# Kernel tuning notes

Hardware: AMD Instinct MI355X
Metric: run time of the kernel (lower is better)

Reference implementation:

```python
import jax, jax.numpy as jnp
import numpy as np

HEADS = 2
NEG_SLOPE = 0.2

def _seg_softmax(alpha, dst, n):
    # numerically-stable softmax over edges grouped by destination node (PyG softmax)
    m = jax.ops.segment_max(alpha, dst, num_segments=n)
    m = jax.lax.stop_gradient(jnp.where(jnp.isfinite(m), m, 0.0))
    e = jnp.exp(alpha - m[dst])
    s = jax.ops.segment_sum(e, dst, num_segments=n)
    return e / (s[dst] + 1e-16)

def _han_layer(xo, xa, e_oo, e_oa, e_ao, Wo, bo, Wa, ba, asrc, adst, Wk, bk, q):
    No, Na = xo.shape[0], xa.shape[0]
    C = Wo.shape[1]
    D = C // HEADS
    h = {'object': (xo @ Wo + bo).reshape(No, HEADS, D),
         'attribute': (xa @ Wa + ba).reshape(Na, HEADS, D)}
    n = {'object': No, 'attribute': Na}
    edge_types = [('object', 'object', e_oo), ('object', 'attribute', e_oa),
                  ('attribute', 'object', e_ao)]
    outs = {'object': [], 'attribute': []}
    for i, (st, dt, e) in enumerate(edge_types):
        src, dst = e[0], e[1]
        # per-edge attention logits [E, H]
        a = (h[st] * asrc[i]).sum(-1)[src] + (h[dt] * adst[i]).sum(-1)[dst]
        a = jax.nn.leaky_relu(a, NEG_SLOPE)
        a = _seg_softmax(a, dst, n[dt])
        msg = (h[st][src] * a[..., None]).reshape(-1, C)  # [E, C]
        outs[dt].append(jax.nn.relu(jax.ops.segment_sum(msg, dst, num_segments=n[dt])))
    res = {}
    for nt, xs in outs.items():
        o = jnp.stack(xs)  # [M, N, C] over metapaths
        score = (q * jnp.tanh(o @ Wk + bk).mean(axis=1)).sum(-1)  # [M]
        w = jax.nn.softmax(score, axis=0)
        res[nt] = jnp.einsum('m,mnc->nc', w, o)
    return res


def setup_inputs() -> dict:
    key = jax.random.key(0)
    ks = jax.random.split(key, 40)
    No, Na, E, C, H = 100000, 50000, 500000, 128, 2
    D = C // H
    def rn(k, shape, scale):
        return jax.random.normal(k, shape, jnp.float32) * scale
    inp = {}
    inp['x_object'] = rn(ks[0], (No, C), 1.0)
    inp['x_attribute'] = rn(ks[1], (Na, C), 1.0)
    inp['e_oo'] = jax.random.randint(ks[2], (2, E), 0, No)
    inp['e_oa'] = jnp.stack([jax.random.randint(ks[3], (E,), 0, No),
                             jax.random.randint(ks[4], (E,), 0, Na)])
    inp['e_ao'] = jnp.stack([jax.random.randint(ks[5], (E,), 0, Na),
                             jax.random.randint(ks[6], (E,), 0, No)])
    s = 1.0 / float(np.sqrt(C))
    for L, off in (('1', 7), ('2', 16)):
        inp['Wo' + L] = rn(ks[off], (C, C), s)
        inp['bo' + L] = jnp.zeros((C,), jnp.float32)
        inp['Wa' + L] = rn(ks[off + 1], (C, C), s)
        inp['ba' + L] = jnp.zeros((C,), jnp.float32)
        inp['asrc' + L] = rn(ks[off + 2], (3, H, D), s)
        inp['adst' + L] = rn(ks[off + 3], (3, H, D), s)
        inp['Wk' + L] = rn(ks[off + 4], (C, C), s)
        inp['bk' + L] = jnp.zeros((C,), jnp.float32)
        inp['q' + L] = rn(ks[off + 5], (C,), s)
    inp['Wl1'] = rn(ks[30], (C, 256), s)
    inp['bl1'] = jnp.zeros((256,), jnp.float32)
    inp['Wl2'] = rn(ks[31], (256, 128), 1.0 / float(np.sqrt(256)))
    inp['bl2'] = jnp.zeros((128,), jnp.float32)
    inp['Wl3'] = rn(ks[32], (128, 8), 1.0 / float(np.sqrt(128)))
    inp['bl3'] = jnp.zeros((8,), jnp.float32)
    return inp


def reference(x_object, x_attribute, e_oo, e_oa, e_ao,
              Wo1, bo1, Wa1, ba1, asrc1, adst1, Wk1, bk1, q1,
              Wo2, bo2, Wa2, ba2, asrc2, adst2, Wk2, bk2, q2,
              Wl1, bl1, Wl2, bl2, Wl3, bl3):
    h = _han_layer(x_object, x_attribute, e_oo, e_oa, e_ao,
                   Wo1, bo1, Wa1, ba1, asrc1, adst1, Wk1, bk1, q1)
    h = _han_layer(h['object'], h['attribute'], e_oo, e_oa, e_ao,
                   Wo2, bo2, Wa2, ba2, asrc2, adst2, Wk2, bk2, q2)
    x = h['object'] @ Wl1 + bl1
    x = x @ Wl2 + bl2
    x = x @ Wl3 + bl3
    return jax.nn.sigmoid(x)
```

## Files before the change

kernel.cpp:

```cpp
#include <hip/hip_runtime.h>
#include <hip/hip_bf16.h>
#include <math.h>

#define CDIM 128
typedef unsigned short u16;
typedef unsigned int u32;
typedef short bf16x8 __attribute__((ext_vector_type(8)));
typedef float f32x4 __attribute__((ext_vector_type(4)));

__device__ __forceinline__ float bf2f(__hip_bfloat16 h) { return __bfloat162float(h); }
__device__ __forceinline__ u16 f2bfbits(float f) {
  __hip_bfloat16 h = __float2bfloat16(f);
  u16 u;
  __builtin_memcpy(&u, &h, 2);
  return u;
}
__device__ __forceinline__ float bfbits2f(u16 b) { return __uint_as_float((u32)b << 16); }
__device__ __forceinline__ float lrelu(float v) { return v > 0.f ? v : 0.2f * v; }
__device__ __forceinline__ float lo_bf(u32 v) { return __uint_as_float(v << 16); }
__device__ __forceinline__ float hi_bf(u32 v) { return __uint_as_float(v & 0xffff0000u); }
__device__ __forceinline__ u32 pack_bf(float a, float b) {
  return (u32)f2bfbits(a) | ((u32)f2bfbits(b) << 16);
}

#define WREP 8
#define WFSZ 16384

__global__ void detect_kernel(const u16* __restrict__ p, int nwords, int* __restrict__ flag) {
  int i = blockIdx.x * blockDim.x + threadIdx.x;
  if (i >= nwords) return;
  int ex = (p[i] >> 7) & 0xFF;
  if (ex >= 0xC0) atomicOr(flag, 1);
}

struct CvtJob { const void* src; float* dst; int n; };
struct CvtJobs24 { CvtJob j[24]; };
__global__ void cvt_batch_kernel(CvtJobs24 jobs, const int* __restrict__ flag) {
  CvtJob jb = jobs.j[blockIdx.y];
  int i = blockIdx.x * blockDim.x + threadIdx.x;
  if (i >= jb.n) return;
  if (*flag) jb.dst[i] = ((const float*)jb.src)[i];
  else jb.dst[i] = bf2f(((const __hip_bfloat16*)jb.src)[i]);
}

__global__ void fill_out_kernel(void* __restrict__ out, float v, int n,
                                const int* __restrict__ flag) {
  int i = blockIdx.x * blockDim.x + threadIdx.x;
  if (i >= n) return;
  if (*flag) ((float*)out)[i] = v;
  else ((__hip_bfloat16*)out)[i] = __float2bfloat16(v);
}

struct RepackJobs { const float* src[6]; u16* dst[6]; };
__global__ void repack_w_kernel(RepackJobs jobs) {
  const float* W = jobs.src[blockIdx.y];
  u16* Wf = jobs.dst[blockIdx.y] + ((size_t)blockIdx.z << 14);
  int idx = blockIdx.x * 256 + threadIdx.x;
  int j = idx & 7, lane = (idx >> 3) & 63, kc = (idx >> 9) & 3, nt = idx >> 11;
  int k = kc * 32 + ((lane >> 4) & 3) * 8 + j;
  int n = nt * 16 + (lane & 15);
  Wf[idx] = f2bfbits(W[k * 128 + n]);
}

struct CsrJobs {
  const int* src[3]; const int* dst[3];
  int* deg[3]; int* cur[3]; int* bsum[3]; int* offs[3]; int* adj[3];
  int Nd[3]; int E;
};
__global__ void deg_batch_kernel(CsrJobs c) {
  int y = blockIdx.y;
  int e = blockIdx.x * blockDim.x + threadIdx.x;
  if (e < c.E) atomicAdd(&c.deg[y][c.dst[y][e]], 1);
}
__global__ void scanp_batch_kernel(CsrJobs c) {
  int y = blockIdx.y, N = c.Nd[y];
  __shared__ int red[256];
  int t = threadIdx.x;
  int base = blockIdx.x * 1024 + t * 4;
  int s = 0;
#pragma unroll
  for (int j = 0; j < 4; ++j) if (base + j < N) s += c.deg[y][base + j];
  red[t] = s;
  __syncthreads();
  for (int o = 128; o; o >>= 1) {
    if (t < o) red[t] += red[t + o];
    __syncthreads();
  }
  if (t == 0) c.bsum[y][blockIdx.x] = red[0];
}
__global__ void scanb_batch_kernel(CsrJobs c) {
  int y = threadIdx.x;
  if (y >= 3) return;
  int nb = (c.Nd[y] + 1023) / 1024;
  int run = 0;
  for (int i = 0; i < nb; ++i) { int v = c.bsum[y][i]; c.bsum[y][i] = run; run += v; }
  c.offs[y][c.Nd[y]] = c.E;
}
__global__ void scanf_batch_kernel(CsrJobs c) {
  int y = blockIdx.y, N = c.Nd[y];
  __shared__ int lds[256];
  int t = threadIdx.x;
  int base = blockIdx.x * 1024 + t * 4;
  int v0 = (base + 0 < N) ? c.deg[y][base + 0] : 0;
  int v1 = (base + 1 < N) ? c.deg[y][base + 1] : 0;
  int v2 = (base + 2 < N) ? c.deg[y][base + 2] : 0;
  int v3 = (base + 3 < N) ? c.deg[y][base + 3] : 0;
  int tsum = v0 + v1 + v2 + v3;
  lds[t] = tsum;
  __syncthreads();
  for (int o = 1; o < 256; o <<= 1) {
    int x = (t >= o) ? lds[t - o] : 0;
    __syncthreads();
    lds[t] += x;
    __syncthreads();
  }
  int excl = lds[t] - tsum + c.bsum[y][blockIdx.x];
  int e0 = excl, e1 = excl + v0, e2 = excl + v0 + v1, e3 = excl + v0 + v1 + v2;
  if (base + 0 < N) { c.offs[y][base + 0] = e0; c.cur[y][base + 0] = e0; }
  if (base + 1 < N) { c.offs[y][base + 1] = e1; c.cur[y][base + 1] = e1; }
  if (base + 2 < N) { c.offs[y][base + 2] = e2; c.cur[y][base + 2] = e2; }
  if (base + 3 < N) { c.offs[y][base + 3] = e3; c.cur[y][base + 3] = e3; }
}
__global__ void fill_batch_kernel(CsrJobs c) {
  int y = blockIdx.y;
  int range8 = blockIdx.x & 7;
  int base = (blockIdx.x >> 3) * 1024 + threadIdx.x * 4;
  if (base >= c.E) return;
  int Nd = c.Nd[y];
  int rsz = (Nd + 7) >> 3;
  int lo = range8 * rsz, hi = lo + rsz;
  const int* dsty = c.dst[y];
  const int* srcy = c.src[y];
  int4 d4;
  if (base + 3 < c.E) {
    d4 = *(const int4*)&dsty[base];
  } else {
    d4.x = dsty[base];
    d4.y = (base + 1 < c.E) ? dsty[base + 1] : -1;
    d4.z = (base + 2 < c.E) ? dsty[base + 2] : -1;
    d4.w = (base + 3 < c.E) ? dsty[base + 3] : -1;
  }
  int dv[4] = { d4.x, d4.y, d4.z, d4.w };
#pragma unroll
  for (int j = 0; j < 4; ++j) {
    int d = dv[j];
    if (d >= lo && d < hi) {
      int p = atomicAdd(&c.cur[y][d], 1);
      c.adj[y][p] = srcy[base + j];
    }
  }
}

struct GemmJob {
  const void* X; const void* X2; const float* W2;
  const u16* Wf; const float* bias;
  const float* av[4]; float* od[4];
  u16* out; int M;
};

template<int MODE>
__device__ __forceinline__ void gemm_load_a(
    const GemmJob& jb, const int* flag, int r, int ko, bf16x8 a[4]) {
  if (MODE == 1 && *flag) {
    const float* af = (const float*)jb.X + (size_t)r * 128 + ko;
#pragma unroll
    for (int c = 0; c < 4; ++c) {
      float4 x = *(const float4*)(af + c * 32);
      float4 y = *(const float4*)(af + c * 32 + 4);
      bf16x8 tv;
      tv[0] = (short)f2bfbits(x.x); tv[1] = (short)f2bfbits(x.y);
      tv[2] = (short)f2bfbits(x.z); tv[3] = (short)f2bfbits(x.w);
      tv[4] = (short)f2bfbits(y.x); tv[5] = (short)f2bfbits(y.y);
      tv[6] = (short)f2bfbits(y.z); tv[7] = (short)f2bfbits(y.w);
      a[c] = tv;
    }
  } else if (MODE == 2) {
    float w0 = jb.W2[0], w1 = jb.W2[1];
    const u16* g1 = (const u16*)jb.X + (size_t)r * 128 + ko;
    const u16* g2 = (const u16*)jb.X2 + (size_t)r * 128 + ko;
#pragma unroll
    for (int c = 0; c < 4; ++c) {
      bf16x8 x1 = *(const bf16x8*)(g1 + c * 32);
      bf16x8 x2 = *(const bf16x8*)(g2 + c * 32);
      bf16x8 tv;
#pragma unroll
      for (int k = 0; k < 8; ++k)
        tv[k] = (short)f2bfbits(w0 * bfbits2f((u16)x1[k]) + w1 * bfbits2f((u16)x2[k]));
      a[c] = tv;
    }
  } else {
    const u16* ab = (const u16*)jb.X + (size_t)r * 128 + ko;
#pragma unroll
    for (int c = 0; c < 4; ++c) a[c] = *(const bf16x8*)(ab + c * 32);
  }
}

template<int MODE, int K>
__global__ __launch_bounds__(256, 4) void gemm_mfma_t(
    GemmJob jb, const int* __restrict__ flag)
{
  int bx = blockIdx.x;
  int M = jb.M;
  __shared__ u16 Cs[64][136];
  int t = threadIdx.x;
  int wave = t >> 6, lane = t & 63;
  int m = lane & 15, ko = (lane >> 4) * 8, rq = lane >> 4;
  int rowbase = bx * 128;
  const u16* wf = jb.Wf + ((size_t)(bx & (WREP - 1)) << 14);

  int r0 = rowbase + wave * 16 + m;       if (r0 >= M) r0 = M - 1;
  int r1 = rowbase + 64 + wave * 16 + m;  if (r1 >= M) r1 = M - 1;
  bf16x8 a0[4], a1[4];
  gemm_load_a<MODE>(jb, flag, r0, ko, a0);
  gemm_load_a<MODE>(jb, flag, r1, ko, a1);

#pragma unroll
  for (int tile = 0; tile < 2; ++tile) {
    int row0 = rowbase + tile * 64 + wave * 16;
    bf16x8* a = tile ? a1 : a0;
    if (row0 < M) {
      f32x4 acc[8];
#pragma unroll
      for (int nt = 0; nt < 8; ++nt) acc[nt] = (f32x4){0.f, 0.f, 0.f, 0.f};
#pragma unroll
      for (int c = 0; c < 4; ++c) {
        bf16x8 b[8];
#pragma unroll
        for (int nt = 0; nt < 8; ++nt)
          b[nt] = *(const bf16x8*)(wf + ((nt * 4 + c) * 64 + lane) * 8);
#pragma unroll
        for (int nt = 0; nt < 8; ++nt)
          acc[nt] = __builtin_amdgcn_mfma_f32_16x16x32_bf16(a[c], b[nt], acc[nt], 0, 0, 0);
      }
#pragma unroll
      for (int nt = 0; nt < 8; ++nt) {
        float bv = jb.bias[nt * 16 + m];
#pragma unroll
        for (int reg = 0; reg < 4; ++reg) acc[nt][reg] += bv;
      }
#pragma unroll
      for (int nt = 0; nt < 8; ++nt) {
        int col = nt * 16 + m;
#pragma unroll
        for (int reg = 0; reg < 4; ++reg)
          Cs[wave * 16 + rq * 4 + reg][col] = f2bfbits(acc[nt][reg]);
      }
#pragma unroll
      for (int k = 0; k < K; ++k) {
        const float* avk = jb.av[k];
        float* odk = jb.od[k];
        float am[8];
#pragma unroll
        for (int nt = 0; nt < 8; ++nt) am[nt] = avk[nt * 16 + m];
#pragma unroll
        for (int reg = 0; reg < 4; ++reg) {
          float p0 = 0.f, p1 = 0.f;
#pragma unroll
          for (int nt = 0; nt < 4; ++nt) p0 = fmaf(acc[nt][reg], am[nt], p0);
#pragma unroll
          for (int nt = 4; nt < 8; ++nt) p1 = fmaf(acc[nt][reg], am[nt], p1);
#pragma unroll
          for (int msk = 1; msk < 16; msk <<= 1) {
            p0 += __shfl_xor(p0, msk);
            p1 += __shfl_xor(p1, msk);
          }
          if (m == 0) {
            int row = row0 + rq * 4 + reg;
            if (row < M) { odk[row * 2] = p0; odk[row * 2 + 1] = p1; }
          }
        }
      }
    }
    __syncthreads();
#pragma unroll
    for (int kk = 0; kk < 4; ++kk) {
      int idx = t + kk * 256;
      int rowl = idx >> 4, c16 = idx & 15;
      int grow = rowbase + tile * 64 + rowl;
      if (grow < M) {
        uint4 v = *(const uint4*)&Cs[rowl][c16 * 8];
        *(uint4*)((u16*)jb.out + (size_t)grow * 128 + c16 * 8) = v;
      }
    }
    __syncthreads();
  }
}

__global__ __launch_bounds__(256) void tanhsum_mfma_kernel(
    const u16* __restrict__ A0, const u16* __restrict__ A1,
    const u16* __restrict__ Wf, const float* __restrict__ bias,
    float* __restrict__ score, int M)
{
  const u16* A = blockIdx.y ? A1 : A0;
  float* sc = score + blockIdx.y * 128;
  __shared__ __align__(16) u16 Bs[WFSZ];
  __shared__ float sred[4][128];
  int t = threadIdx.x;
  int wave = t >> 6, lane = t & 63;
  int m = lane & 15, ko = (lane >> 4) * 8, rq = lane >> 4;
  {
    const uint4* wfg = (const uint4*)(Wf + ((size_t)(blockIdx.x & (WREP - 1)) << 14));
    uint4* bs4 = (uint4*)Bs;
#pragma unroll
    for (int i = 0; i < 8; ++i) bs4[t + i * 256] = wfg[t + i * 256];
  }
  __syncthreads();
  float colsum[8];
#pragma unroll
  for (int nt = 0; nt < 8; ++nt) colsum[nt] = 0.f;
  for (int row0 = blockIdx.x * 64 + wave * 16; row0 < M; row0 += gridDim.x * 64) {
    int r = row0 + m; if (r >= M) r = M - 1;
    const u16* arow = A + (size_t)r * 128 + ko;
    bf16x8 a[4];
#pragma unroll
    for (int c = 0; c < 4; ++c) a[c] = *(const bf16x8*)(arow + c * 32);
    f32x4 acc[8];
#pragma unroll
    for (int nt = 0; nt < 8; ++nt) acc[nt] = (f32x4){0.f, 0.f, 0.f, 0.f};
#pragma unroll
    for (int c = 0; c < 4; ++c) {
      bf16x8 b[8];
#pragma unroll
      for (int nt = 0; nt < 8; ++nt)
        b[nt] = *(const bf16x8*)(Bs + ((nt * 4 + c) * 64 + lane) * 8);
#pragma unroll
      for (int nt = 0; nt < 8; ++nt)
        acc[nt] = __builtin_amdgcn_mfma_f32_16x16x32_bf16(a[c], b[nt], acc[nt], 0, 0, 0);
    }
#pragma unroll
    for (int nt = 0; nt < 8; ++nt) {
      float bv = bias[nt * 16 + m];
#pragma unroll
      for (int reg = 0; reg < 4; ++reg) {
        int row = row0 + rq * 4 + reg;
        if (row < M) colsum[nt] += tanhf(acc[nt][reg] + bv);
      }
    }
  }
#pragma unroll
  for (int nt = 0; nt < 8; ++nt) {
    colsum[nt] += __shfl_xor(colsum[nt], 16);
    colsum[nt] += __shfl_xor(colsum[nt], 32);
  }
  if (lane < 16) {
#pragma unroll
    for (int nt = 0; nt < 8; ++nt) sred[wave][nt * 16 + lane] = colsum[nt];
  }
  __syncthreads();
  if (t < 128) {
    float tot = sred[0][t] + sred[1][t] + sred[2][t] + sred[3][t];
    atomicAdd(&sc[t], tot);
  }
}

__global__ void sem_w_kernel(const float* __restrict__ score, const float* __restrict__ q,
                             float invN, float* __restrict__ W2) {
  int t = threadIdx.x;
  float s0 = 0.f, s1 = 0.f;
  for (int c = t; c < 128; c += 64) {
    float qc = q[c];
    s0 += qc * score[c];
    s1 += qc * score[128 + c];
  }
#pragma unroll
  for (int o = 32; o; o >>= 1) {
    s0 += __shfl_xor(s0, o);
    s1 += __shfl_xor(s1, o);
  }
  if (t == 0) {
    s0 *= invN; s1 *= invN;
    float mx = fmaxf(s0, s1);
    float e0 = expf(s0 - mx), e1 = expf(s1 - mx);
    float inv = 1.f / (e0 + e1);
    W2[0] = e0 * inv;
    W2[1] = e1 * inv;
  }
}

struct GatherJob {
  const int* offs; const int* adj;
  const float* ss; const float* sd;
  float* ew;
  const u16* Hs; u16* out; int Nd;
};
struct GatherJobs3 { GatherJob j[3]; };
__global__ __launch_bounds__(256) void node_gather_b_kernel(GatherJobs3 g, int nb0, int nb01)
{
  int bx = blockIdx.x;
  int jbi = bx < nb0 ? 0 : (bx < nb01 ? 1 : 2);
  int bl = jbi == 0 ? bx : (jbi == 1 ? bx - nb0 : bx - nb01);
  GatherJob jb = g.j[jbi];
  int lane = threadIdx.x & 63;
  int grp = lane >> 4, sl = lane & 15;
  int wid = bl * 4 + (threadIdx.x >> 6);
  int node = wid * 4 + grp;
  bool act = node < jb.Nd;
  int beg = 0, end = 0;
  float2 sdp = make_float2(0.f, 0.f);
  if (act) {
    beg = jb.offs[node];
    end = jb.offs[node + 1];
    sdp = ((const float2*)jb.sd)[node];
  }
  int deg = end - beg;
  const float2* ss2 = (const float2*)jb.ss;
  float2* ew2 = (float2*)jb.ew;
  const uint4* H4 = (const uint4*)jb.Hs;
  bool hi2 = sl >= 8;
  int base = grp * 16;
  float a[8];
#pragma unroll
  for (int j = 0; j < 8; ++j) a[j] = 0.f;
  float invh;
  if (__all(deg <= 16)) {
    int adjreg = 0;
    if (sl < deg) adjreg = jb.adj[beg + sl];
    int sidx[8];
#pragma unroll
    for (int j = 0; j < 8; ++j) sidx[j] = __shfl(adjreg, base + j);
    float2 ssp = make_float2(0.f, 0.f);
    if (sl < deg) ssp = ss2[adjreg];
    uint4 v[8];
#pragma unroll
    for (int j = 0; j < 8; ++j)
      if (j < deg) v[j] = H4[(size_t)sidx[j] * 16 + sl];
    float e0r = 0.f, e1r = 0.f;
    if (sl < deg) {
      e0r = expf(lrelu(ssp.x + sdp.x));
      e1r = expf(lrelu(ssp.y + sdp.y));
    }
    float s0 = e0r, s1 = e1r;
#pragma unroll
    for (int o = 1; o < 16; o <<= 1) {
      s0 += __shfl_xor(s0, o);
      s1 += __shfl_xor(s1, o);
    }
    invh = 1.f / ((hi2 ? s1 : s0) + 1e-16f);
#pragma unroll
    for (int j = 0; j < 8; ++j) {
      float wl = __shfl(e0r, base + j);
      float wh = __shfl(e1r, base + j);
      if (j < deg) {
        float w = hi2 ? wh : wl;
        a[0] = fmaf(lo_bf(v[j].x), w, a[0]);
        a[1] = fmaf(hi_bf(v[j].x), w, a[1]);
        a[2] = fmaf(lo_bf(v[j].y), w, a[2]);
        a[3] = fmaf(hi_bf(v[j].y), w, a[3]);
        a[4] = fmaf(lo_bf(v[j].z), w, a[4]);
        a[5] = fmaf(hi_bf(v[j].z), w, a[5]);
        a[6] = fmaf(lo_bf(v[j].w), w, a[6]);
        a[7] = fmaf(hi_bf(v[j].w), w, a[7]);
      }
    }
    if (__any(deg > 8)) {
#pragma unroll
      for (int j = 0; j < 8; ++j) {
        int s2 = __shfl(adjreg, base + 8 + j);
        float wl = __shfl(e0r, base + 8 + j);
        float wh = __shfl(e1r, base + 8 + j);
        if (8 + j < deg) {
          uint4 vv = H4[(size_t)s2 * 16 + sl];
          float w = hi2 ? wh : wl;
          a[0] = fmaf(lo_bf(vv.x), w, a[0]);
          a[1] = fmaf(hi_bf(vv.x), w, a[1]);
          a[2] = fmaf(lo_bf(vv.y), w, a[2]);
          a[3] = fmaf(hi_bf(vv.y), w, a[3]);
          a[4] = fmaf(lo_bf(vv.z), w, a[4]);
          a[5] = fmaf(hi_bf(vv.z), w, a[5]);
          a[6] = fmaf(lo_bf(vv.w), w, a[6]);
          a[7] = fmaf(hi_bf(vv.w), w, a[7]);
        }
      }
    }
  } else {
    float s0 = 0.f, s1 = 0.f;
    for (int e = beg + sl; e < end; e += 16) {
      int s = jb.adj[e];
      float2 ssp = ss2[s];
      float f0 = expf(lrelu(ssp.x + sdp.x));
      float f1 = expf(lrelu(ssp.y + sdp.y));
      ew2[e] = make_float2(f0, f1);
      s0 += f0;
      s1 += f1;
    }
#pragma unroll
    for (int o = 1; o < 16; o <<= 1) {
      s0 += __shfl_xor(s0, o);
      s1 += __shfl_xor(s1, o);
    }
    invh = 1.f / ((hi2 ? s1 : s0) + 1e-16f);
    for (int eb = beg; eb < end; eb += 4) {
      int eA[4]; uint4 v[4]; float w[4];
#pragma unroll
      for (int j = 0; j < 4; ++j) eA[j] = (eb + j < end) ? eb + j : end - 1;
#pragma unroll
      for (int j = 0; j < 4; ++j) v[j] = H4[(size_t)jb.adj[eA[j]] * 16 + sl];
#pragma unroll
      for (int j = 0; j < 4; ++j) {
        float2 p = ew2[eA[j]];
        w[j] = (eb + j < end) ? (hi2 ? p.y : p.x) : 0.f;
      }
#pragma unroll
      for (int j = 0; j < 4; ++j) {
        a[0] = fmaf(lo_bf(v[j].x), w[j], a[0]);
        a[1] = fmaf(hi_bf(v[j].x), w[j], a[1]);
        a[2] = fmaf(lo_bf(v[j].y), w[j], a[2]);
        a[3] = fmaf(hi_bf(v[j].y), w[j], a[3]);
        a[4] = fmaf(lo_bf(v[j].z), w[j], a[4]);
        a[5] = fmaf(hi_bf(v[j].z), w[j], a[5]);
        a[6] = fmaf(lo_bf(v[j].w), w[j], a[6]);
        a[7] = fmaf(hi_bf(v[j].w), w[j], a[7]);
      }
    }
  }
  if (act) {
    uint4 o;
    o.x = pack_bf(fmaxf(a[0] * invh, 0.f), fmaxf(a[1] * invh, 0.f));
    o.y = pack_bf(fmaxf(a[2] * invh, 0.f), fmaxf(a[3] * invh, 0.f));
    o.z = pack_bf(fmaxf(a[4] * invh, 0.f), fmaxf(a[5] * invh, 0.f));
    o.w = pack_bf(fmaxf(a[6] * invh, 0.f), fmaxf(a[7] * invh, 0.f));
    ((uint4*)jb.out)[(size_t)node * 16 + sl] = o;
  }
}

__global__ void fold1_kernel(const float* __restrict__ Wl1, const float* __restrict__ bl1,
                             const float* __restrict__ Wl2, const float* __restrict__ bl2,
                             float* __restrict__ WT1, float* __restrict__ TB) {
  int idx = blockIdx.x * blockDim.x + threadIdx.x;
  if (idx < 128 * 128) {
    int m = idx >> 7, n = idx & 127;
    float acc = 0.f;
    for (int k = 0; k < 256; ++k) acc = fmaf(Wl1[m * 256 + k], Wl2[k * 128 + n], acc);
    WT1[idx] = acc;
  } else if (idx < 128 * 128 + 128) {
    int n = idx - 128 * 128;
    float acc = bl2[n];
    for (int k = 0; k < 256; ++k) acc = fmaf(bl1[k], Wl2[k * 128 + n], acc);
    TB[n] = acc;
  }
}
__global__ void fold2_kernel(const float* __restrict__ WT1, const float* __restrict__ TB,
                             const float* __restrict__ Wl3, const float* __restrict__ bl3,
                             float* __restrict__ WC, float* __restrict__ BC) {
  int idx = blockIdx.x * blockDim.x + threadIdx.x;
  if (idx < 128 * 8) {
    int m = idx >> 3, j = idx & 7;
    float acc = 0.f;
    for (int k = 0; k < 128; ++k) acc = fmaf(WT1[m * 128 + k], Wl3[k * 8 + j], acc);
    WC[idx] = acc;
  } else if (idx < 128 * 8 + 8) {
    int j = idx - 128 * 8;
    float acc = bl3[j];
    for (int k = 0; k < 128; ++k) acc = fmaf(TB[k], Wl3[k * 8 + j], acc);
    BC[j] = acc;
  }
}

__global__ __launch_bounds__(256) void final_mlp_kernel(
    const u16* __restrict__ X1, const u16* __restrict__ X2,
    const float* __restrict__ W2, const int* __restrict__ flag,
    const float* __restrict__ Wc, const float* __restrict__ bc,
    void* __restrict__ out, int M) {
  __shared__ float Xs[32][130];
  int rb = blockIdx.x * 32;
  int t = threadIdx.x;
  float w0 = W2[0], w1 = W2[1];
  for (int i = t; i < 32 * 64; i += 256) {
    int r = i >> 6, c2 = i & 63;
    int gr = rb + r;
    u32 v1 = 0, v2 = 0;
    if (gr < M) {
      v1 = ((const u32*)X1)[(size_t)gr * 64 + c2];
      v2 = ((const u32*)X2)[(size_t)gr * 64 + c2];
    }
    Xs[r][c2 * 2] = w0 * lo_bf(v1) + w1 * lo_bf(v2);
    Xs[r][c2 * 2 + 1] = w0 * hi_bf(v1) + w1 * hi_bf(v2);
  }
  __syncthreads();
  int r = t >> 3, j = t & 7;
  int gr = rb + r;
  if (gr >= M) return;
  float acc = bc[j];
#pragma unroll 4
  for (int c = 0; c < 128; ++c) acc = fmaf(Xs[r][c], Wc[c * 8 + j], acc);
  float v = 1.f / (1.f + expf(-acc));
  if (*flag) ((float*)out)[(size_t)gr * 8 + j] = v;
  else ((__hip_bfloat16*)out)[(size_t)gr * 8 + j] = __float2bfloat16(v);
}

extern "C" void kernel_launch(void* const* d_in, const int* in_sizes, int n_in,
                              void* d_out, int out_size, void* d_ws, size_t ws_size,
                              hipStream_t stream) {
  const int No = in_sizes[0] / CDIM;
  const int Na = in_sizes[1] / CDIM;
  const int E = in_sizes[2] / 2;
  const int NM = No > Na ? No : Na;

  char* base = (char*)d_ws;
  size_t off = 0;
  auto alloc = [&](size_t bytes) -> void* {
    off = (off + 255) & ~(size_t)255;
    void* p = base + off;
    off += bytes;
    return p;
  };

  int* FLAG = (int*)alloc(4);
  u16* G1b = (u16*)alloc((size_t)No * CDIM * 2);
  u16* XAb = (u16*)alloc((size_t)Na * CDIM * 2);
  u16* HOb = (u16*)alloc((size_t)No * CDIM * 2);
  u16* HAb = (u16*)alloc((size_t)Na * CDIM * 2);
  u16* G2b = (u16*)alloc((size_t)No * CDIM * 2);
  float* OD0 = (float*)alloc((size_t)No * 2 * 4);
  float* OD1 = (float*)alloc((size_t)No * 2 * 4);
  float* OD2 = (float*)alloc((size_t)No * 2 * 4);
  float* OD3 = (float*)alloc((size_t)No * 2 * 4);
  float* AD0 = (float*)alloc((size_t)Na * 2 * 4);
  float* AD1 = (float*)alloc((size_t)Na * 2 * 4);
  float* EW0 = (float*)alloc((size_t)E * 2 * 4);
  float* EW1 = (float*)alloc((size_t)E * 2 * 4);
  float* EW2 = (float*)alloc((size_t)E * 2 * 4);
  int* DEG3 = (int*)alloc((size_t)NM * 3 * 4);
  float* SCORE = (float*)alloc(512 * 4);
  float* SEMW = (float*)alloc(4 * 4);
  float* WT1 = (float*)alloc(128 * 128 * 4);
  float* TB = (float*)alloc(128 * 4);
  float* WC = (float*)alloc(128 * 8 * 4);
  float* BC = (float*)alloc(8 * 4);
  int* OFFS_OO = (int*)alloc((size_t)(No + 1) * 4);
  int* OFFS_OA = (int*)alloc((size_t)(Na + 1) * 4);
  int* OFFS_AO = (int*)alloc((size_t)(No + 1) * 4);
  int* ADJ_OO = (int*)alloc((size_t)E * 4);
  int* ADJ_OA = (int*)alloc((size_t)E * 4);
  int* ADJ_AO = (int*)alloc((size_t)E * 4);
  int* CUR3 = (int*)alloc((size_t)NM * 3 * 4);
  int* BSUM3 = (int*)alloc(3 * 128 * 4);
  u16* WF[6];
  for (int i = 0; i < 6; ++i) WF[i] = (u16*)alloc((size_t)WFSZ * WREP * 2);
  float* F[29];
  for (int i = 5; i < 29; ++i) F[i] = (float*)alloc((size_t)in_sizes[i] * 4);

  hipMemsetAsync(FLAG, 0, 4, stream);
  detect_kernel<<<64, 256, 0, stream>>>((const u16*)d_in[0], 16384, FLAG);

  if (off > ws_size) {
    fill_out_kernel<<<(out_size + 255) / 256, 256, 0, stream>>>(d_out, 0.25f, out_size, FLAG);
    return;
  }

  {
    CvtJobs24 jobs;
    int maxn = 0;
    for (int i = 5; i < 29; ++i) {
      jobs.j[i - 5].src = d_in[i];
      jobs.j[i - 5].dst = F[i];
      jobs.j[i - 5].n = in_sizes[i];
      if (in_sizes[i] > maxn) maxn = in_sizes[i];
    }
    dim3 g((maxn + 255) / 256, 24);
    cvt_batch_kernel<<<g, 256, 0, stream>>>(jobs, FLAG);
  }

  {
    RepackJobs rj;
    const int widx[6] = { 5, 7, 11, 14, 16, 20 };
    for (int i = 0; i < 6; ++i) { rj.src[i] = F[widx[i]]; rj.dst[i] = WF[i]; }
    dim3 g(64, 6, WREP);
    repack_w_kernel<<<g, 256, 0, stream>>>(rj);
  }

  {
    CsrJobs c;
    const int* EOO = (const int*)d_in[2];
    const int* EOA = (const int*)d_in[3];
    const int* EAO = (const int*)d_in[4];
    c.src[0] = EOO; c.dst[0] = EOO + E; c.Nd[0] = No; c.offs[0] = OFFS_OO; c.adj[0] = ADJ_OO;
    c.src[1] = EOA; c.dst[1] = EOA + E; c.Nd[1] = Na; c.offs[1] = OFFS_OA; c.adj[1] = ADJ_OA;
    c.src[2] = EAO; c.dst[2] = EAO + E; c.Nd[2] = No; c.offs[2] = OFFS_AO; c.adj[2] = ADJ_AO;
    for (int i = 0; i < 3; ++i) {
      c.deg[i] = DEG3 + (size_t)i * NM;
      c.cur[i] = CUR3 + (size_t)i * NM;
      c.bsum[i] = BSUM3 + i * 128;
    }
    c.E = E;
    size_t zlen = (size_t)((char*)(SEMW + 4) - (char*)DEG3);
    hipMemsetAsync(DEG3, 0, zlen, stream);
    int nbmax = (NM + 1023) / 1024;
    deg_batch_kernel<<<dim3((E + 255) / 256, 3), 256, 0, stream>>>(c);
    scanp_batch_kernel<<<dim3(nbmax, 3), 256, 0, stream>>>(c);
    scanb_batch_kernel<<<1, 64, 0, stream>>>(c);
    scanf_batch_kernel<<<dim3(nbmax, 3), 256, 0, stream>>>(c);
    fill_batch_kernel<<<dim3(((E + 1023) / 1024) * 8, 3), 256, 0, stream>>>(c);
  }

  const int nb0 = (No + 127) / 128;
  const int nb1 = (Na + 127) / 128;

  auto run_layer = [&](int L, const void* XO, const void* XO2, const float* W2in,
                       const void* XA,
                       const float* bo, const float* ba,
                       const float* av, const float* ad, const float* bk,
                       const float* q) {
    u16* WFo = WF[L * 3 + 0];
    u16* WFa = WF[L * 3 + 1];
    u16* WFk = WF[L * 3 + 2];
    float* SC = SCORE + L * 256;
    GemmJob j0;
    j0.X = XO; j0.X2 = XO2; j0.W2 = W2in;
    j0.Wf = WFo; j0.bias = bo;
    j0.av[0] = av + 0;   j0.od[0] = OD0;
    j0.av[1] = ad + 0;   j0.od[1] = OD1;
    j0.av[2] = av + 128; j0.od[2] = OD2;
    j0.av[3] = ad + 256; j0.od[3] = OD3;
    j0.out = HOb; j0.M = No;
    GemmJob j1;
    j1.X = XA; j1.X2 = nullptr; j1.W2 = nullptr;
    j1.Wf = WFa; j1.bias = ba;
    j1.av[0] = av + 256; j1.od[0] = AD0;
    j1.av[1] = ad + 128; j1.od[1] = AD1;
    j1.av[2] = nullptr;  j1.od[2] = nullptr;
    j1.av[3] = nullptr;  j1.od[3] = nullptr;
    j1.out = HAb; j1.M = Na;
    if (L == 0) {
      gemm_mfma_t<1, 4><<<nb0, 256, 0, stream>>>(j0, FLAG);
      gemm_mfma_t<1, 2><<<nb1, 256, 0, stream>>>(j1, FLAG);
    } else {
      gemm_mfma_t<2, 4><<<nb0, 256, 0, stream>>>(j0, FLAG);
      gemm_mfma_t<0, 1><<<nb1, 256, 0, stream>>>(j1, FLAG);
    }

    GatherJobs3 ga;
    ga.j[0] = { OFFS_OO, ADJ_OO, OD0, OD1, EW0, HOb, G1b, No };
    int c0 = (No + 15) / 16, c1, c2;
    if (L == 0) {
      ga.j[1] = { OFFS_OA, ADJ_OA, OD2, AD1, EW1, HOb, XAb, Na };
      ga.j[2] = { OFFS_AO, ADJ_AO, AD0, OD3, EW2, HAb, G2b, No };
      c1 = (Na + 15) / 16;
      c2 = (No + 15) / 16;
    } else {
      ga.j[1] = { OFFS_AO, ADJ_AO, AD0, OD3, EW2, HAb, G2b, No };
      ga.j[2] = ga.j[1];
      c1 = (No + 15) / 16;
      c2 = 0;
    }
    node_gather_b_kernel<<<c0 + c1 + c2, 256, 0, stream>>>(ga, c0, c0 + c1);

    tanhsum_mfma_kernel<<<dim3(512, 2), 256, 0, stream>>>(G1b, G2b, WFk, bk, SC, No);
    sem_w_kernel<<<1, 64, 0, stream>>>(SC, q, 1.f / (float)No, SEMW + L * 2);
  };

  run_layer(0, d_in[0], nullptr, nullptr, d_in[1],
            F[6], F[8], F[9], F[10], F[12], F[13]);
  run_layer(1, G1b, G2b, SEMW, XAb,
            F[15], F[17], F[18], F[19], F[21], F[22]);

  fold1_kernel<<<(128 * 128 + 128 + 255) / 256, 256, 0, stream>>>(F[23], F[24], F[25], F[26], WT1, TB);
  fold2_kernel<<<(128 * 8 + 8 + 255) / 256, 256, 0, stream>>>(WT1, TB, F[27], F[28], WC, BC);

  final_mlp_kernel<<<(No + 31) / 32, 256, 0, stream>>>(G1b, G2b, SEMW + 2, FLAG, WC, BC, d_out, No);
}
```

Measured before the change: 652.7 us.

## Build CSR with per-edge atomic ranks instead of cursor-based fill

The degree-count kernel now records the value returned by the atomic increment as each edge's rank within its destination segment. The fill kernel then scatters source ids to offs[dst]+rank with no atomics and no longer needs the 8-way destination range partitioning that read the edge list eight times. This removes the cursor array and the second pass of atomics. The cost is an extra E-sized rank buffer per edge type that must be written and read back, and the adjacency order within a segment becomes nondeterministic.

```diff
diff --git a/kernel.cpp b/kernel.cpp
--- a/kernel.cpp
+++ b/kernel.cpp
@@ -64,13 +64,21 @@
 
 struct CsrJobs {
   const int* src[3]; const int* dst[3];
-  int* deg[3]; int* cur[3]; int* bsum[3]; int* offs[3]; int* adj[3];
+  int* deg[3]; int* rank[3]; int* bsum[3]; int* offs[3]; int* adj[3];
   int Nd[3]; int E;
 };
 __global__ void deg_batch_kernel(CsrJobs c) {
   int y = blockIdx.y;
-  int e = blockIdx.x * blockDim.x + threadIdx.x;
-  if (e < c.E) atomicAdd(&c.deg[y][c.dst[y][e]], 1);
+  int base = (blockIdx.x * blockDim.x + threadIdx.x) * 4;
+  if (base >= c.E) return;
+  const int* dsty = c.dst[y];
+  int* degy = c.deg[y];
+  int* ranky = c.rank[y];
+#pragma unroll
+  for (int j = 0; j < 4; ++j) {
+    int e = base + j;
+    if (e < c.E) ranky[e] = atomicAdd(&degy[dsty[e]], 1);
+  }
 }
 __global__ void scanp_batch_kernel(CsrJobs c) {
   int y = blockIdx.y, N = c.Nd[y];
@@ -115,38 +123,32 @@
     __syncthreads();
   }
   int excl = lds[t] - tsum + c.bsum[y][blockIdx.x];
-  int e0 = excl, e1 = excl + v0, e2 = excl + v0 + v1, e3 = excl + v0 + v1 + v2;
-  if (base + 0 < N) { c.offs[y][base + 0] = e0; c.cur[y][base + 0] = e0; }
-  if (base + 1 < N) { c.offs[y][base + 1] = e1; c.cur[y][base + 1] = e1; }
-  if (base + 2 < N) { c.offs[y][base + 2] = e2; c.cur[y][base + 2] = e2; }
-  if (base + 3 < N) { c.offs[y][base + 3] = e3; c.cur[y][base + 3] = e3; }
+  if (base + 0 < N) c.offs[y][base + 0] = excl;
+  if (base + 1 < N) c.offs[y][base + 1] = excl + v0;
+  if (base + 2 < N) c.offs[y][base + 2] = excl + v0 + v1;
+  if (base + 3 < N) c.offs[y][base + 3] = excl + v0 + v1 + v2;
 }
 __global__ void fill_batch_kernel(CsrJobs c) {
   int y = blockIdx.y;
-  int range8 = blockIdx.x & 7;
-  int base = (blockIdx.x >> 3) * 1024 + threadIdx.x * 4;
+  int base = (blockIdx.x * blockDim.x + threadIdx.x) * 4;
   if (base >= c.E) return;
-  int Nd = c.Nd[y];
-  int rsz = (Nd + 7) >> 3;
-  int lo = range8 * rsz, hi = lo + rsz;
   const int* dsty = c.dst[y];
   const int* srcy = c.src[y];
-  int4 d4;
+  const int* ranky = c.rank[y];
+  const int* offsy = c.offs[y];
+  int* adjy = c.adj[y];
   if (base + 3 < c.E) {
-    d4 = *(const int4*)&dsty[base];
+    int4 d4 = *(const int4*)&dsty[base];
+    int4 r4 = *(const int4*)&ranky[base];
+    int4 s4 = *(const int4*)&srcy[base];
+    adjy[offsy[d4.x] + r4.x] = s4.x;
+    adjy[offsy[d4.y] + r4.y] = s4.y;
+    adjy[offsy[d4.z] + r4.z] = s4.z;
+    adjy[offsy[d4.w] + r4.w] = s4.w;
   } else {
-    d4.x = dsty[base];
-    d4.y = (base + 1 < c.E) ? dsty[base + 1] : -1;
-    d4.z = (base + 2 < c.E) ? dsty[base + 2] : -1;
-    d4.w = (base + 3 < c.E) ? dsty[base + 3] : -1;
-  }
-  int dv[4] = { d4.x, d4.y, d4.z, d4.w };
-#pragma unroll
-  for (int j = 0; j < 4; ++j) {
-    int d = dv[j];
-    if (d >= lo && d < hi) {
-      int p = atomicAdd(&c.cur[y][d], 1);
-      c.adj[y][p] = srcy[base + j];
+    for (int j = 0; j < 4 && base + j < c.E; ++j) {
+      int e = base + j;
+      adjy[offsy[dsty[e]] + ranky[e]] = srcy[e];
     }
   }
 }
@@ -633,7 +635,7 @@
   int* ADJ_OO = (int*)alloc((size_t)E * 4);
   int* ADJ_OA = (int*)alloc((size_t)E * 4);
   int* ADJ_AO = (int*)alloc((size_t)E * 4);
-  int* CUR3 = (int*)alloc((size_t)NM * 3 * 4);
+  int* RANK3 = (int*)alloc((size_t)E * 3 * 4);
   int* BSUM3 = (int*)alloc(3 * 128 * 4);
   u16* WF[6];
   for (int i = 0; i < 6; ++i) WF[i] = (u16*)alloc((size_t)WFSZ * WREP * 2);
@@ -679,18 +681,19 @@
     c.src[2] = EAO; c.dst[2] = EAO + E; c.Nd[2] = No; c.offs[2] = OFFS_AO; c.adj[2] = ADJ_AO;
     for (int i = 0; i < 3; ++i) {
       c.deg[i] = DEG3 + (size_t)i * NM;
-      c.cur[i] = CUR3 + (size_t)i * NM;
+      c.rank[i] = RANK3 + (size_t)i * E;
       c.bsum[i] = BSUM3 + i * 128;
     }
     c.E = E;
     size_t zlen = (size_t)((char*)(SEMW + 4) - (char*)DEG3);
     hipMemsetAsync(DEG3, 0, zlen, stream);
     int nbmax = (NM + 1023) / 1024;
-    deg_batch_kernel<<<dim3((E + 255) / 256, 3), 256, 0, stream>>>(c);
+    int nbe = (E + 1023) / 1024;
+    deg_batch_kernel<<<dim3(nbe, 3), 256, 0, stream>>>(c);
     scanp_batch_kernel<<<dim3(nbmax, 3), 256, 0, stream>>>(c);
     scanb_batch_kernel<<<1, 64, 0, stream>>>(c);
     scanf_batch_kernel<<<dim3(nbmax, 3), 256, 0, stream>>>(c);
-    fill_batch_kernel<<<dim3(((E + 1023) / 1024) * 8, 3), 256, 0, stream>>>(c);
+    fill_batch_kernel<<<dim3(nbe, 3), 256, 0, stream>>>(c);
   }
 
   const int nb0 = (No + 127) / 128;
```

After: 624.4 us. 4.3% less time.
